# Performance work log

Hardware: AMD Instinct MI355X
Metric: run time of the kernel (lower is better)

Reference implementation:

```python
import jax, jax.numpy as jnp
import numpy as np

E, H, V = 512, 1024, 32000
T_IN, T_DEC, B = 128, 128, 64
SOS = 1
WIPE_IDS = jnp.array([2, 3, 4])  # <EOS>, '\u56fe', '\u6298'


def gru_cell(x, h, Wih, Whh, bih, bhh):
    # torch nn.GRU cell math
    gi = x @ Wih.T + bih  # [B, 3H]
    gh = h @ Whh.T + bhh  # [B, 3H]
    i_r, i_z, i_n = jnp.split(gi, 3, axis=-1)
    h_r, h_z, h_n = jnp.split(gh, 3, axis=-1)
    r = jax.nn.sigmoid(i_r + h_r)
    z = jax.nn.sigmoid(i_z + h_z)
    n = jnp.tanh(i_n + r * h_n)
    return (1.0 - z) * n + z * h


def setup_inputs() -> dict:
    key = jax.random.key(0)
    ks = jax.random.split(key, 20)
    f = lambda k, shape: jax.random.normal(k, shape, jnp.float32) * 0.05
    inp = {
        'emb': f(ks[0], (V, E)),
        'enc_Wih': f(ks[1], (3 * H, E)), 'enc_Whh': f(ks[2], (3 * H, H)),
        'enc_bih': f(ks[3], (3 * H,)), 'enc_bhh': f(ks[4], (3 * H,)),
        'attn_W': f(ks[5], (T_IN, E + H)), 'attn_b': f(ks[6], (T_IN,)),
        'comb_W': f(ks[7], (H, E + H)), 'comb_b': f(ks[8], (H,)),
        'dec_Wih': f(ks[9], (3 * H, H)), 'dec_Whh': f(ks[10], (3 * H, H)),
        'dec_bih': f(ks[11], (3 * H,)), 'dec_bhh': f(ks[12], (3 * H,)),
        'out_W': f(ks[13], (V, H)), 'out_b': f(ks[14], (V,)),
        'src_tokens': jax.random.randint(ks[15], (B, T_IN), 0, V, jnp.int32),
        'tgt_tokens': jax.random.randint(ks[16], (B, T_DEC), 0, V, jnp.int32),
    }
    # pack_padded_sequence needs lengths sorted descending with max == T_IN
    sl = jax.random.randint(ks[17], (B,), 1, T_IN + 1, jnp.int32).at[0].set(T_IN)
    inp['src_lengths'] = jnp.sort(sl)[::-1]
    tl = jax.random.randint(ks[18], (B,), 1, T_DEC + 1, jnp.int32).at[0].set(T_DEC)
    inp['tgt_lengths'] = tl
    return inp


def reference(emb, enc_Wih, enc_Whh, enc_bih, enc_bhh, attn_W, attn_b,
              comb_W, comb_b, dec_Wih, dec_Whh, dec_bih, dec_bhh,
              out_W, out_b, src_tokens, src_lengths, tgt_tokens, tgt_lengths):
    # ---------------- Encoder (packed GRU semantics) ----------------
    x = emb[src_tokens]  # [B, T_IN, E]  (dropout is eval-mode identity)
    valid = jnp.arange(T_IN)[None, :] < src_lengths[:, None]  # [B, T_IN]

    def enc_step(h, inp):
        xt, vt = inp  # [B,E], [B]
        hn = gru_cell(xt, h, enc_Wih, enc_Whh, enc_bih, enc_bhh)
        h = jnp.where(vt[:, None], hn, h)          # freeze hidden past length
        out = jnp.where(vt[:, None], hn, 0.0)      # pad_packed zeros past length
        return h, out

    h0 = jnp.zeros((B, H), emb.dtype)
    enc_h, enc_out = jax.lax.scan(enc_step, h0, (x.transpose(1, 0, 2), valid.T))
    enc_out = enc_out.transpose(1, 0, 2)  # [B, T_IN, H]
    enc_out = jax.nn.log_softmax(enc_out, axis=1)  # LogSoftmax(dim=1) over time, as in source

    # ---------------- Attention decoder with teacher forcing ----------------
    sos = jnp.full((B,), SOS, src_tokens.dtype)

    def dec_step(carry, inp):
        h, prev = carry
        di, tgt_t = inp
        e = emb[prev]  # [B, E]
        union = jnp.concatenate([e, h], axis=-1)  # [B, E+H]
        aw = jax.nn.softmax(union @ attn_W.T + attn_b, axis=-1)  # [B, T_IN]
        info = jnp.einsum('bt,bth->bh', aw, enc_out)  # bmm
        comb = jax.nn.relu(jnp.concatenate([e, info], axis=-1) @ comb_W.T + comb_b)
        h = gru_cell(comb, h, dec_Wih, dec_Whh, dec_bih, dec_bhh)
        logits = h @ out_W.T + out_b  # [B, V]
        m = di < tgt_lengths  # [B] wipeEOS condition: now_len < length[i]
        wiped = jnp.where(m[:, None], 0.0, logits[:, WIPE_IDS])
        logits = logits.at[:, WIPE_IDS].set(wiped)
        pred_t = jnp.argmax(logits, axis=-1)
        ce = -jax.nn.log_softmax(logits, axis=-1)[jnp.arange(B), tgt_t]
        mf = m.astype(logits.dtype)
        step_loss = jnp.sum(ce * mf) / jnp.sum(mf)  # masked_select(...).mean()
        return (h, tgt_t), (pred_t, step_loss)

    (_, _), (preds, losses) = jax.lax.scan(
        dec_step, (enc_h, sos), (jnp.arange(T_DEC), tgt_tokens.T))
    return preds.T, jnp.sum(losses)
```

## Files before the change

### kernel.cpp

```cpp
#include <hip/hip_runtime.h>
#include <math.h>

typedef long long i64;

#define B_    64
#define TIN   128
#define TDEC  128
#define E_    512
#define H_    1024
#define V_    32000
#define H3    3072
#define EH    1536
#define NROWS 8192
#define BH    (B_ * H_)

__device__ inline unsigned int ordf(float v) {
  unsigned int u = __float_as_uint(v);
  return (u & 0x80000000u) ? ~u : (u | 0x80000000u);
}

__device__ __forceinline__ void fma16(float acc[4][4], float4 s, float4 w) {
  acc[0][0] = fmaf(s.x, w.x, acc[0][0]); acc[0][1] = fmaf(s.x, w.y, acc[0][1]);
  acc[0][2] = fmaf(s.x, w.z, acc[0][2]); acc[0][3] = fmaf(s.x, w.w, acc[0][3]);
  acc[1][0] = fmaf(s.y, w.x, acc[1][0]); acc[1][1] = fmaf(s.y, w.y, acc[1][1]);
  acc[1][2] = fmaf(s.y, w.z, acc[1][2]); acc[1][3] = fmaf(s.y, w.w, acc[1][3]);
  acc[2][0] = fmaf(s.z, w.x, acc[2][0]); acc[2][1] = fmaf(s.z, w.y, acc[2][1]);
  acc[2][2] = fmaf(s.z, w.z, acc[2][2]); acc[2][3] = fmaf(s.z, w.w, acc[2][3]);
  acc[3][0] = fmaf(s.w, w.x, acc[3][0]); acc[3][1] = fmaf(s.w, w.y, acc[3][1]);
  acc[3][2] = fmaf(s.w, w.z, acc[3][2]); acc[3][3] = fmaf(s.w, w.w, acc[3][3]);
}

__global__ void diag_fill(float* __restrict__ out, int n, float val) {
  int i = blockIdx.x * blockDim.x + threadIdx.x;
  if (i < n) out[i] = val;
}

__global__ void init_ws(float* __restrict__ hbuf, unsigned long long* __restrict__ amaxkey,
                        float* __restrict__ sumexp) {
  int i = blockIdx.x * blockDim.x + threadIdx.x;
  if (i < 2 * B_ * H_) hbuf[i] = 0.f;
  if (i < NROWS) { amaxkey[i] = 0ull; sumexp[i] = 0.f; }
}

__global__ void prep_tokens(const int* __restrict__ src, const int* __restrict__ tgt,
                            int* __restrict__ tok_src, int* __restrict__ tok_prev) {
  int r = blockIdx.x * blockDim.x + threadIdx.x;
  if (r >= NROWS) return;
  int t = r >> 6, b = r & 63;
  tok_src[r]  = src[b * TIN + t];
  tok_prev[r] = (t == 0) ? 1 : tgt[b * TDEC + (t - 1)];
}

__global__ __launch_bounds__(256)
void gemm_gather(const float* __restrict__ emb, const int* __restrict__ tok,
                 const float* __restrict__ W, int wstride,
                 const float* __restrict__ bias,
                 float* __restrict__ C, int ldc) {
  __shared__ float As[32][132];
  __shared__ float Bs[32][136];
  __shared__ int toks[128];
  const int tid = threadIdx.x;
  const int tx = tid & 15, ty = tid >> 4;
  const int r0 = blockIdx.y * 128, n0 = blockIdx.x * 128;
  if (tid < 128) toks[tid] = tok[r0 + tid];
  __syncthreads();
  float acc[8][8];
#pragma unroll
  for (int i = 0; i < 8; ++i)
#pragma unroll
    for (int j = 0; j < 8; ++j) acc[i][j] = 0.f;

  for (int k0 = 0; k0 < E_; k0 += 32) {
#pragma unroll
    for (int j = 0; j < 4; ++j) {
      int s = tid + 256 * j;
      int m = s >> 3, k4 = (s & 7) << 2;
      float4 v = *reinterpret_cast<const float4*>(&emb[(i64)toks[m] * E_ + k0 + k4]);
      As[k4 + 0][m] = v.x; As[k4 + 1][m] = v.y; As[k4 + 2][m] = v.z; As[k4 + 3][m] = v.w;
      float4 u = *reinterpret_cast<const float4*>(&W[(i64)(n0 + m) * wstride + k0 + k4]);
      Bs[k4 + 0][m] = u.x; Bs[k4 + 1][m] = u.y; Bs[k4 + 2][m] = u.z; Bs[k4 + 3][m] = u.w;
    }
    __syncthreads();
#pragma unroll
    for (int k = 0; k < 32; ++k) {
      float a[8], b[8];
      *(float4*)&a[0] = *(float4*)&As[k][ty * 4];
      *(float4*)&a[4] = *(float4*)&As[k][64 + ty * 4];
      *(float4*)&b[0] = *(float4*)&Bs[k][tx * 4];
      *(float4*)&b[4] = *(float4*)&Bs[k][64 + tx * 4];
#pragma unroll
      for (int i = 0; i < 8; ++i)
#pragma unroll
        for (int j = 0; j < 8; ++j)
          acc[i][j] = fmaf(a[i], b[j], acc[i][j]);
    }
    __syncthreads();
  }
#pragma unroll
  for (int i = 0; i < 8; ++i) {
    int rl = (i < 4) ? (ty * 4 + i) : (64 + ty * 4 + i - 4);
    int r = r0 + rl;
#pragma unroll
    for (int j = 0; j < 8; ++j) {
      int cl = (j < 4) ? (tx * 4 + j) : (64 + tx * 4 + j - 4);
      int c = n0 + cl;
      C[(i64)r * ldc + c] = acc[i][j] + bias[c];
    }
  }
}

__global__ __launch_bounds__(512)
void enc_step2(const float* __restrict__ h_prev, float* __restrict__ h_next,
               const float* __restrict__ emb, const int* __restrict__ tokS,
               const float* __restrict__ Wih, const float* __restrict__ Whh,
               const float* __restrict__ bih, const float* __restrict__ bhh,
               const int* __restrict__ src_len, float* __restrict__ EncRaw, int t) {
  __shared__ float S[64][68];
  __shared__ float WL[64 * 32];
  __shared__ float red[8 * 1024];
  __shared__ int toks[64];
  const int tid = threadIdx.x;
  const int n0 = blockIdx.x * 4;
  const int bg = tid & 15, ac = (tid >> 4) & 3, ks = tid >> 6;
  const int b0 = bg * 4;
  if (tid < 64) toks[tid] = tokS[t * B_ + tid];
  float acc[4][4] = {{0}};
  for (int ch = 0; ch < 24; ++ch) {
    const bool isE = ch < 8;
    const int k0 = (isE ? ch : ch - 8) * 64;
    __syncthreads();
    {
      int b = tid & 63, kb = (tid >> 6) * 8;
      const float* src = isE ? &emb[(i64)toks[b] * E_ + k0 + kb]
                             : &h_prev[(i64)b * H_ + k0 + kb];
      float4 v0 = *(const float4*)src;
      float4 v1 = *(const float4*)(src + 4);
      S[kb + 0][b] = v0.x; S[kb + 1][b] = v0.y; S[kb + 2][b] = v0.z; S[kb + 3][b] = v0.w;
      S[kb + 4][b] = v1.x; S[kb + 5][b] = v1.y; S[kb + 6][b] = v1.z; S[kb + 7][b] = v1.w;
    }
    if (tid < 192) {
      int lin = tid * 4;
      int row12 = lin >> 6, k4 = lin & 63;
      int m = row12 >> 2, c = row12 & 3;
      const float* W = isE ? Wih : Whh;
      const int K = isE ? E_ : H_;
      float4 w = *(const float4*)&W[(i64)(m * H_ + n0 + c) * K + k0 + k4];
      int slot = ((m ^ ((k4 >> 2) & 7)) << 2) + c;
      WL[(k4 + 0) * 32 + slot] = w.x;
      WL[(k4 + 1) * 32 + slot] = w.y;
      WL[(k4 + 2) * 32 + slot] = w.z;
      WL[(k4 + 3) * 32 + slot] = w.w;
    }
    __syncthreads();
    const bool active = (ac < 2) || (ac == 2 && isE) || (ac == 3 && !isE);
    if (active) {
      const int m = (ac < 2) ? ac : 2;
#pragma unroll
      for (int kk = ks * 8; kk < ks * 8 + 8; ++kk) {
        float4 sv = *(float4*)&S[kk][b0];
        float4 wv = *(float4*)&WL[kk * 32 + ((m ^ ((kk >> 2) & 7)) << 2)];
        fma16(acc, sv, wv);
      }
    }
  }
  __syncthreads();
#pragma unroll
  for (int bi = 0; bi < 4; ++bi)
#pragma unroll
    for (int c = 0; c < 4; ++c)
      red[ks * 1024 + ac * 256 + c * 64 + b0 + bi] = acc[bi][c];
  __syncthreads();
  if (tid < 256) {
    int b = tid & 63, c = tid >> 6, col = n0 + c;
    float sr = 0, sz = 0, gin = 0, ghn = 0;
#pragma unroll
    for (int k2 = 0; k2 < 8; ++k2) {
      sr  += red[k2 * 1024 +   0 + c * 64 + b];
      sz  += red[k2 * 1024 + 256 + c * 64 + b];
      gin += red[k2 * 1024 + 512 + c * 64 + b];
      ghn += red[k2 * 1024 + 768 + c * 64 + b];
    }
    float r = 1.f / (1.f + expf(-(sr + bih[col] + bhh[col])));
    float z = 1.f / (1.f + expf(-(sz + bih[H_ + col] + bhh[H_ + col])));
    float nn = tanhf(gin + bih[2 * H_ + col] + r * (ghn + bhh[2 * H_ + col]));
    float hpv = h_prev[(i64)b * H_ + col];
    float hnew = (1.f - z) * nn + z * hpv;
    bool valid = t < src_len[b];
    h_next[(i64)b * H_ + col] = valid ? hnew : hpv;
    EncRaw[((i64)b * TIN + t) * H_ + col] = valid ? hnew : 0.f;
  }
}

__global__ void ls_time(float* __restrict__ Enc) {
  int idx = blockIdx.x * blockDim.x + threadIdx.x;
  int b = idx >> 10, c = idx & 1023;
  const i64 base = (i64)b * TIN * H_ + c;
  float M = -INFINITY;
  for (int t = 0; t < TIN; ++t) M = fmaxf(M, Enc[base + (i64)t * H_]);
  float S = 0.f;
  for (int t = 0; t < TIN; ++t) S += expf(Enc[base + (i64)t * H_] - M);
  float lg = M + logf(S);
  for (int t = 0; t < TIN; ++t) Enc[base + (i64)t * H_] -= lg;
}

__global__ __launch_bounds__(512)
void attn_info2(const float* __restrict__ h_prev, const float* __restrict__ Ae,
                const float* __restrict__ attn_W, const float* __restrict__ EncLS,
                float* __restrict__ info, int t) {
  __shared__ float hl[H_];
  __shared__ float sc[TIN];
  __shared__ float inf2[512];
  const int b = blockIdx.x & 63, quarter = blockIdx.x >> 6;
  const int tid = threadIdx.x;
  if (tid < 256) {
    float4 v = *(const float4*)&h_prev[(i64)b * H_ + tid * 4];
    *(float4*)&hl[tid * 4] = v;
  }
  __syncthreads();
  const int w = tid >> 6, lane = tid & 63;
#pragma unroll
  for (int si = 0; si < 16; ++si) {
    int s = w * 16 + si;
    float p = 0.f;
#pragma unroll
    for (int jj = 0; jj < 16; ++jj) {
      int j = jj * 64 + lane;
      p = fmaf(hl[j], attn_W[(i64)s * EH + E_ + j], p);
    }
#pragma unroll
    for (int off = 32; off > 0; off >>= 1) p += __shfl_down(p, off);
    if (lane == 0) sc[s] = p + Ae[((i64)t * B_ + b) * TIN + s];
  }
  __syncthreads();
  if (tid < 64) {
    float v0 = sc[tid], v1 = sc[tid + 64];
    float mx = fmaxf(v0, v1);
#pragma unroll
    for (int off = 32; off > 0; off >>= 1) mx = fmaxf(mx, __shfl_xor(mx, off));
    float e0 = expf(v0 - mx), e1 = expf(v1 - mx);
    float ss = e0 + e1;
#pragma unroll
    for (int off = 32; off > 0; off >>= 1) ss += __shfl_xor(ss, off);
    sc[tid] = e0 / ss; sc[tid + 64] = e1 / ss;
  }
  __syncthreads();
  {
    int c = quarter * 256 + (tid & 255);
    int th = tid >> 8;
    float acc = 0.f;
    for (int t2 = th * 64; t2 < th * 64 + 64; ++t2)
      acc = fmaf(sc[t2], EncLS[((i64)b * TIN + t2) * H_ + c], acc);
    inf2[tid] = acc;
    __syncthreads();
    if (th == 0) info[(i64)b * H_ + c] = acc + inf2[tid + 256];
  }
}

__global__ __launch_bounds__(512)
void comb2(const float* __restrict__ info, const float* __restrict__ emb,
           const int* __restrict__ tokP, const float* __restrict__ comb_W,
           const float* __restrict__ comb_b, float* __restrict__ comb, int t) {
  __shared__ float S[64][68];
  __shared__ float WB[64 * 20];
  __shared__ float red[8 * 256];
  __shared__ int toks[64];
  const int tid = threadIdx.x;
  const int n0 = blockIdx.x * 4;
  const int bg = tid & 15, cs = (tid >> 4) & 3, ks = tid >> 6;
  const int b0 = bg * 4;
  if (tid < 64) toks[tid] = tokP[t * B_ + tid];
  float acc[4] = {0, 0, 0, 0};
  for (int ch = 0; ch < 24; ++ch) {
    const bool isE = ch < 8;
    const int k0 = (isE ? ch : ch - 8) * 64;
    __syncthreads();
    {
      int b = tid & 63, kb = (tid >> 6) * 8;
      const float* src = isE ? &emb[(i64)toks[b] * E_ + k0 + kb]
                             : &info[(i64)b * H_ + k0 + kb];
      float4 v0 = *(const float4*)src;
      float4 v1 = *(const float4*)(src + 4);
      S[kb + 0][b] = v0.x; S[kb + 1][b] = v0.y; S[kb + 2][b] = v0.z; S[kb + 3][b] = v0.w;
      S[kb + 4][b] = v1.x; S[kb + 5][b] = v1.y; S[kb + 6][b] = v1.z; S[kb + 7][b] = v1.w;
    }
    if (tid < 64) {
      int k = tid;
      i64 koff = (i64)(isE ? 0 : E_) + k0 + k;
      float4 w;
      w.x = comb_W[(i64)(n0 + 0) * EH + koff];
      w.y = comb_W[(i64)(n0 + 1) * EH + koff];
      w.z = comb_W[(i64)(n0 + 2) * EH + koff];
      w.w = comb_W[(i64)(n0 + 3) * EH + koff];
      *(float4*)&WB[k * 20] = w;
    }
    __syncthreads();
#pragma unroll
    for (int kk = ks * 8; kk < ks * 8 + 8; ++kk) {
      float4 sv = *(float4*)&S[kk][b0];
      float wv = WB[kk * 20 + cs];
      acc[0] = fmaf(sv.x, wv, acc[0]);
      acc[1] = fmaf(sv.y, wv, acc[1]);
      acc[2] = fmaf(sv.z, wv, acc[2]);
      acc[3] = fmaf(sv.w, wv, acc[3]);
    }
  }
  __syncthreads();
#pragma unroll
  for (int bi = 0; bi < 4; ++bi)
    red[ks * 256 + cs * 64 + b0 + bi] = acc[bi];
  __syncthreads();
  if (tid < 256) {
    int b = tid & 63, c = tid >> 6;
    float s = comb_b[n0 + c];
#pragma unroll
    for (int k2 = 0; k2 < 8; ++k2) s += red[k2 * 256 + c * 64 + b];
    comb[(i64)b * H_ + n0 + c] = fmaxf(s, 0.f);
  }
}

__global__ __launch_bounds__(512)
void dec_gru2(const float* __restrict__ h_prev, const float* __restrict__ comb,
              const float* __restrict__ Wih, const float* __restrict__ Whh,
              const float* __restrict__ bih, const float* __restrict__ bhh,
              float* __restrict__ h_out) {
  __shared__ float S1[64][68];
  __shared__ float S2[64][68];
  __shared__ float WL[64 * 32];
  __shared__ float red[8 * 1024];
  const int tid = threadIdx.x;
  const int n0 = blockIdx.x * 4;
  const int bg = tid & 15, ac = (tid >> 4) & 3, ks = tid >> 6;
  const int b0 = bg * 4;
  float acc[4][4] = {{0}};
  for (int ch = 0; ch < 16; ++ch) {
    const int k0 = ch * 64;
    __syncthreads();
    {
      int b = tid & 63, kb = (tid >> 6) * 8;
      const float* s1 = &h_prev[(i64)b * H_ + k0 + kb];
      const float* s2 = &comb[(i64)b * H_ + k0 + kb];
      float4 v0 = *(const float4*)s1, v1 = *(const float4*)(s1 + 4);
      S1[kb + 0][b] = v0.x; S1[kb + 1][b] = v0.y; S1[kb + 2][b] = v0.z; S1[kb + 3][b] = v0.w;
      S1[kb + 4][b] = v1.x; S1[kb + 5][b] = v1.y; S1[kb + 6][b] = v1.z; S1[kb + 7][b] = v1.w;
      float4 u0 = *(const float4*)s2, u1 = *(const float4*)(s2 + 4);
      S2[kb + 0][b] = u0.x; S2[kb + 1][b] = u0.y; S2[kb + 2][b] = u0.z; S2[kb + 3][b] = u0.w;
      S2[kb + 4][b] = u1.x; S2[kb + 5][b] = u1.y; S2[kb + 6][b] = u1.z; S2[kb + 7][b] = u1.w;
    }
    if (tid < 384) {
      int lin = tid * 4;
      int row24 = lin >> 6, k4 = lin & 63;
      int m = row24 >> 2, c = row24 & 3;
      int g = m >> 1;
      const float* W = (m & 1) ? Wih : Whh;
      float4 w = *(const float4*)&W[(i64)(g * H_ + n0 + c) * H_ + k0 + k4];
      int slot = ((m ^ ((k4 >> 2) & 7)) << 2) + c;
      WL[(k4 + 0) * 32 + slot] = w.x;
      WL[(k4 + 1) * 32 + slot] = w.y;
      WL[(k4 + 2) * 32 + slot] = w.z;
      WL[(k4 + 3) * 32 + slot] = w.w;
    }
    __syncthreads();
    if (ac < 2) {
#pragma unroll
      for (int kk = ks * 8; kk < ks * 8 + 8; ++kk) {
        int key = (kk >> 2) & 7;
        float4 h4 = *(float4*)&S1[kk][b0];
        float4 c4 = *(float4*)&S2[kk][b0];
        float4 wh = *(float4*)&WL[kk * 32 + (((2 * ac) ^ key) << 2)];
        float4 wi = *(float4*)&WL[kk * 32 + (((2 * ac + 1) ^ key) << 2)];
        fma16(acc, h4, wh);
        fma16(acc, c4, wi);
      }
    } else if (ac == 2) {
#pragma unroll
      for (int kk = ks * 8; kk < ks * 8 + 8; ++kk) {
        int key = (kk >> 2) & 7;
        float4 c4 = *(float4*)&S2[kk][b0];
        float4 wi = *(float4*)&WL[kk * 32 + ((5 ^ key) << 2)];
        fma16(acc, c4, wi);
      }
    } else {
#pragma unroll
      for (int kk = ks * 8; kk < ks * 8 + 8; ++kk) {
        int key = (kk >> 2) & 7;
        float4 h4 = *(float4*)&S1[kk][b0];
        float4 wh = *(float4*)&WL[kk * 32 + ((4 ^ key) << 2)];
        fma16(acc, h4, wh);
      }
    }
  }
  __syncthreads();
#pragma unroll
  for (int bi = 0; bi < 4; ++bi)
#pragma unroll
    for (int c = 0; c < 4; ++c)
      red[ks * 1024 + ac * 256 + c * 64 + b0 + bi] = acc[bi][c];
  __syncthreads();
  if (tid < 256) {
    int b = tid & 63, c = tid >> 6, col = n0 + c;
    float sr = 0, sz = 0, gin = 0, ghn = 0;
#pragma unroll
    for (int k2 = 0; k2 < 8; ++k2) {
      sr  += red[k2 * 1024 +   0 + c * 64 + b];
      sz  += red[k2 * 1024 + 256 + c * 64 + b];
      gin += red[k2 * 1024 + 512 + c * 64 + b];
      ghn += red[k2 * 1024 + 768 + c * 64 + b];
    }
    float r = 1.f / (1.f + expf(-(sr + bih[col] + bhh[col])));
    float z = 1.f / (1.f + expf(-(sz + bih[H_ + col] + bhh[H_ + col])));
    float nn = tanhf(gin + bih[2 * H_ + col] + r * (ghn + bhh[2 * H_ + col]));
    float hpv = h_prev[(i64)b * H_ + col];
    h_out[(i64)b * H_ + col] = (1.f - z) * nn + z * hpv;
  }
}

__global__ __launch_bounds__(256)
void logits_fused(const float* __restrict__ A, const float* __restrict__ Wout,
                  const float* __restrict__ outb, const int* __restrict__ tlen,
                  unsigned long long* __restrict__ amaxkey, float* __restrict__ sumexp) {
  __shared__ union {
    struct { float As[32][132]; float Bs[32][136]; } g;
    struct { float redm[128][17]; int redi[128][17]; float reds[128][17]; } r;
  } sh;
  const int tid = threadIdx.x;
  const int tx = tid & 15, ty = tid >> 4;
  const int r0 = blockIdx.y * 128, n0 = blockIdx.x * 128;
  float acc[8][8];
#pragma unroll
  for (int i = 0; i < 8; ++i)
#pragma unroll
    for (int j = 0; j < 8; ++j) acc[i][j] = 0.f;

  for (int k0 = 0; k0 < H_; k0 += 32) {
#pragma unroll
    for (int j = 0; j < 4; ++j) {
      int s = tid + 256 * j;
      int m = s >> 3, k4 = (s & 7) << 2;
      float4 v = *reinterpret_cast<const float4*>(&A[(i64)(r0 + m) * H_ + k0 + k4]);
      sh.g.As[k4 + 0][m] = v.x; sh.g.As[k4 + 1][m] = v.y;
      sh.g.As[k4 + 2][m] = v.z; sh.g.As[k4 + 3][m] = v.w;
      float4 u = *reinterpret_cast<const float4*>(&Wout[(i64)(n0 + m) * H_ + k0 + k4]);
      sh.g.Bs[k4 + 0][m] = u.x; sh.g.Bs[k4 + 1][m] = u.y;
      sh.g.Bs[k4 + 2][m] = u.z; sh.g.Bs[k4 + 3][m] = u.w;
    }
    __syncthreads();
#pragma unroll
    for (int k = 0; k < 32; ++k) {
      float a[8], b[8];
      *(float4*)&a[0] = *(float4*)&sh.g.As[k][ty * 4];
      *(float4*)&a[4] = *(float4*)&sh.g.As[k][64 + ty * 4];
      *(float4*)&b[0] = *(float4*)&sh.g.Bs[k][tx * 4];
      *(float4*)&b[4] = *(float4*)&sh.g.Bs[k][64 + tx * 4];
#pragma unroll
      for (int i = 0; i < 8; ++i)
#pragma unroll
        for (int j = 0; j < 8; ++j)
          acc[i][j] = fmaf(a[i], b[j], acc[i][j]);
    }
    __syncthreads();
  }

  int cols[8], rloc[8];
#pragma unroll
  for (int j = 0; j < 8; ++j) cols[j] = n0 + ((j < 4) ? (tx * 4 + j) : (64 + tx * 4 + j - 4));
#pragma unroll
  for (int i = 0; i < 8; ++i) rloc[i] = (i < 4) ? (ty * 4 + i) : (64 + ty * 4 + i - 4);

#pragma unroll
  for (int i = 0; i < 8; ++i) {
    int r = r0 + rloc[i];
    int t = r >> 6, b = r & 63;
    bool m = t < tlen[b];
    float lm = -INFINITY; int li = 0x7fffffff; float ls = 0.f;
#pragma unroll
    for (int j = 0; j < 8; ++j) {
      float v = acc[i][j] + outb[cols[j]];
      if (m && cols[j] >= 2 && cols[j] <= 4) v = 0.f;
      ls += expf(v);
      if (v > lm || (v == lm && cols[j] < li)) { lm = v; li = cols[j]; }
    }
    sh.r.redm[rloc[i]][tx] = lm; sh.r.redi[rloc[i]][tx] = li; sh.r.reds[rloc[i]][tx] = ls;
  }
  __syncthreads();
  if (tid < 128) {
    float M = -INFINITY; int I = 0x7fffffff; float S = 0.f;
#pragma unroll
    for (int x = 0; x < 16; ++x) {
      float v = sh.r.redm[tid][x]; int id = sh.r.redi[tid][x];
      if (v > M || (v == M && id < I)) { M = v; I = id; }
      S += sh.r.reds[tid][x];
    }
    unsigned long long key = ((unsigned long long)ordf(M) << 32) | (0xFFFFFFFFu - (unsigned)I);
    atomicMax(&amaxkey[r0 + tid], key);
    atomicAdd(&sumexp[r0 + tid], S);
  }
}

__global__ void tlogit_kernel(const float* __restrict__ Hd, const float* __restrict__ Wout,
                              const float* __restrict__ outb, const int* __restrict__ tgt,
                              const int* __restrict__ tlen, float* __restrict__ tlog) {
  const int tid = threadIdx.x;
  const int w = tid >> 6, lane = tid & 63;
  const int r = blockIdx.x * 4 + w;
  const int t = r >> 6, b = r & 63;
  const int tg = tgt[b * TDEC + t];
  float p = 0.f;
#pragma unroll
  for (int jj = 0; jj < 16; ++jj) {
    int j = jj * 64 + lane;
    p = fmaf(Hd[(i64)r * H_ + j], Wout[(i64)tg * H_ + j], p);
  }
#pragma unroll
  for (int off = 32; off > 0; off >>= 1) p += __shfl_down(p, off);
  if (lane == 0) {
    float v = p + outb[tg];
    if ((t < tlen[b]) && tg >= 2 && tg <= 4) v = 0.f;
    tlog[r] = v;
  }
}

__global__ void merge_kernel(const unsigned long long* __restrict__ amaxkey,
                             const float* __restrict__ sumexp,
                             const float* __restrict__ tlog,
                             const int* __restrict__ tlen,
                             float* __restrict__ out, float* __restrict__ loss_t) {
  const int t = blockIdx.x, b = threadIdx.x;
  const int r = t * 64 + b;
  unsigned long long key = amaxkey[r];
  int I = (int)(0xFFFFFFFFu - (unsigned)(key & 0xFFFFFFFFull));
  float lse = logf(sumexp[r]);
  float ce = lse - tlog[r];
  bool m = t < tlen[b];
  out[b * TDEC + t] = (float)I;
  float num = m ? ce : 0.f;
  float den = m ? 1.f : 0.f;
#pragma unroll
  for (int off = 32; off > 0; off >>= 1) {
    num += __shfl_down(num, off);
    den += __shfl_down(den, off);
  }
  if (b == 0) loss_t[t] = num / den;
}

__global__ void loss_sum(const float* __restrict__ loss_t, float* __restrict__ out) {
  const int tid = threadIdx.x;
  float v = loss_t[tid];
#pragma unroll
  for (int off = 32; off > 0; off >>= 1) v += __shfl_down(v, off);
  __shared__ float ps[2];
  if ((tid & 63) == 0) ps[tid >> 6] = v;
  __syncthreads();
  if (tid == 0) out[B_ * TDEC] = ps[0] + ps[1];
}

extern "C" void kernel_launch(void* const* d_in, const int* in_sizes, int n_in,
                              void* d_out, int out_size, void* d_ws, size_t ws_size,
                              hipStream_t stream) {
  const float* emb     = (const float*)d_in[0];
  const float* enc_Wih = (const float*)d_in[1];
  const float* enc_Whh = (const float*)d_in[2];
  const float* enc_bih = (const float*)d_in[3];
  const float* enc_bhh = (const float*)d_in[4];
  const float* attn_W  = (const float*)d_in[5];
  const float* attn_b  = (const float*)d_in[6];
  const float* comb_W  = (const float*)d_in[7];
  const float* comb_b  = (const float*)d_in[8];
  const float* dec_Wih = (const float*)d_in[9];
  const float* dec_Whh = (const float*)d_in[10];
  const float* dec_bih = (const float*)d_in[11];
  const float* dec_bhh = (const float*)d_in[12];
  const float* out_W   = (const float*)d_in[13];
  const float* out_b   = (const float*)d_in[14];
  const int* src_tok = (const int*)d_in[15];
  const int* tgt_tok;
  const int* src_len;
  const int* tgt_len;
  if (in_sizes[16] == B_ * TDEC) {
    tgt_tok = (const int*)d_in[16];
    src_len = (const int*)d_in[17];
    tgt_len = (const int*)d_in[18];
  } else {
    src_len = (const int*)d_in[16];
    tgt_len = (const int*)d_in[17];
    tgt_tok = (const int*)d_in[18];
  }
  float* out = (float*)d_out;
  char* wsb = (char*)d_ws;
  size_t off = 0;
  auto alloc = [&](size_t bytes) { void* p = wsb + off; off += (bytes + 255) & ~(size_t)255; return p; };

  float* EncLS = (float*)alloc((size_t)NROWS * H_ * 4);
  float* hbuf  = (float*)alloc(2ull * B_ * H_ * 4);
  float* Ae    = (float*)alloc((size_t)NROWS * TIN * 4);
  float* Hdec  = (float*)alloc((size_t)NROWS * H_ * 4);
  float* info  = (float*)alloc((size_t)B_ * H_ * 4);
  float* comb  = (float*)alloc((size_t)B_ * H_ * 4);
  unsigned long long* amaxkey = (unsigned long long*)alloc((size_t)NROWS * 8);
  float* sumexp = (float*)alloc((size_t)NROWS * 4);
  float* tlog  = (float*)alloc((size_t)NROWS * 4);
  float* lossT = (float*)alloc(TDEC * 4);
  int* tokS    = (int*)alloc(NROWS * 4);
  int* tokP    = (int*)alloc(NROWS * 4);

  if (off > ws_size) {
    diag_fill<<<(out_size + 255) / 256, 256, 0, stream>>>(out, out_size, (float)ws_size);
    return;
  }

  init_ws<<<512, 256, 0, stream>>>(hbuf, amaxkey, sumexp);
  prep_tokens<<<32, 256, 0, stream>>>(src_tok, tgt_tok, tokS, tokP);
  gemm_gather<<<dim3(1, 64), 256, 0, stream>>>(emb, tokP, attn_W, EH, attn_b, Ae, TIN);

  for (int t = 0; t < TIN; ++t) {
    const float* hp = hbuf + (size_t)(t & 1) * BH;
    float* hn = hbuf + (size_t)((t + 1) & 1) * BH;
    enc_step2<<<256, 512, 0, stream>>>(hp, hn, emb, tokS, enc_Wih, enc_Whh,
                                       enc_bih, enc_bhh, src_len, EncLS, t);
  }
  ls_time<<<256, 256, 0, stream>>>(EncLS);

  for (int t = 0; t < TDEC; ++t) {
    const float* hp = (t == 0) ? hbuf : (Hdec + (i64)(t - 1) * BH);
    attn_info2<<<256, 512, 0, stream>>>(hp, Ae, attn_W, EncLS, info, t);
    comb2<<<256, 512, 0, stream>>>(info, emb, tokP, comb_W, comb_b, comb, t);
    dec_gru2<<<256, 512, 0, stream>>>(hp, comb, dec_Wih, dec_Whh, dec_bih, dec_bhh,
                                      Hdec + (i64)t * BH);
  }

  logits_fused<<<dim3(250, 64), 256, 0, stream>>>(Hdec, out_W, out_b, tgt_len, amaxkey, sumexp);
  tlogit_kernel<<<2048, 256, 0, stream>>>(Hdec, out_W, out_b, tgt_tok, tgt_len, tlog);
  merge_kernel<<<128, 64, 0, stream>>>(amaxkey, sumexp, tlog, tgt_len, out, lossT);
  loss_sum<<<1, 128, 0, stream>>>(lossT, out);
}
```

Before: 36.11 ms.

## Precompute embedding part of combine projection as batched GEMM; union shared memory

The embedding half of the comb_W projection depends only on teacher-forced tokens, so it is computed once for all decoder steps by a batched gather-GEMM into a workspace buffer Ce. Each per-step comb2 launch then covers only the info half (16 chunks instead of 24) and adds the precomputed value. Shared-memory arrays in the step kernels are overlaid with unions to cut LDS usage, and nontemporal loads are used for EncLS and out_W streams. This costs an extra 32MB workspace buffer and one upfront GEMM, and falls back to the old path if the workspace is too small.

```diff
diff --git a/kernel.cpp b/kernel.cpp
--- a/kernel.cpp
+++ b/kernel.cpp
@@ -2,6 +2,7 @@
 #include <math.h>
 
 typedef long long i64;
+typedef float f32x4 __attribute__((ext_vector_type(4)));
 
 #define B_    64
 #define TIN   128
@@ -115,15 +116,15 @@
                const float* __restrict__ Wih, const float* __restrict__ Whh,
                const float* __restrict__ bih, const float* __restrict__ bhh,
                const int* __restrict__ src_len, float* __restrict__ EncRaw, int t) {
-  __shared__ float S[64][68];
-  __shared__ float WL[64 * 32];
-  __shared__ float red[8 * 1024];
-  __shared__ int toks[64];
+  __shared__ union {
+    struct { float S[64][68]; float WL[64 * 32]; int toks[64]; } m;
+    float red[8 * 1024];
+  } sh;
   const int tid = threadIdx.x;
   const int n0 = blockIdx.x * 4;
   const int bg = tid & 15, ac = (tid >> 4) & 3, ks = tid >> 6;
   const int b0 = bg * 4;
-  if (tid < 64) toks[tid] = tokS[t * B_ + tid];
+  if (tid < 64) sh.m.toks[tid] = tokS[t * B_ + tid];
   float acc[4][4] = {{0}};
   for (int ch = 0; ch < 24; ++ch) {
     const bool isE = ch < 8;
@@ -131,12 +132,14 @@
     __syncthreads();
     {
       int b = tid & 63, kb = (tid >> 6) * 8;
-      const float* src = isE ? &emb[(i64)toks[b] * E_ + k0 + kb]
+      const float* src = isE ? &emb[(i64)sh.m.toks[b] * E_ + k0 + kb]
                              : &h_prev[(i64)b * H_ + k0 + kb];
       float4 v0 = *(const float4*)src;
       float4 v1 = *(const float4*)(src + 4);
-      S[kb + 0][b] = v0.x; S[kb + 1][b] = v0.y; S[kb + 2][b] = v0.z; S[kb + 3][b] = v0.w;
-      S[kb + 4][b] = v1.x; S[kb + 5][b] = v1.y; S[kb + 6][b] = v1.z; S[kb + 7][b] = v1.w;
+      sh.m.S[kb + 0][b] = v0.x; sh.m.S[kb + 1][b] = v0.y;
+      sh.m.S[kb + 2][b] = v0.z; sh.m.S[kb + 3][b] = v0.w;
+      sh.m.S[kb + 4][b] = v1.x; sh.m.S[kb + 5][b] = v1.y;
+      sh.m.S[kb + 6][b] = v1.z; sh.m.S[kb + 7][b] = v1.w;
     }
     if (tid < 192) {
       int lin = tid * 4;
@@ -146,10 +149,10 @@
       const int K = isE ? E_ : H_;
       float4 w = *(const float4*)&W[(i64)(m * H_ + n0 + c) * K + k0 + k4];
       int slot = ((m ^ ((k4 >> 2) & 7)) << 2) + c;
-      WL[(k4 + 0) * 32 + slot] = w.x;
-      WL[(k4 + 1) * 32 + slot] = w.y;
-      WL[(k4 + 2) * 32 + slot] = w.z;
-      WL[(k4 + 3) * 32 + slot] = w.w;
+      sh.m.WL[(k4 + 0) * 32 + slot] = w.x;
+      sh.m.WL[(k4 + 1) * 32 + slot] = w.y;
+      sh.m.WL[(k4 + 2) * 32 + slot] = w.z;
+      sh.m.WL[(k4 + 3) * 32 + slot] = w.w;
     }
     __syncthreads();
     const bool active = (ac < 2) || (ac == 2 && isE) || (ac == 3 && !isE);
@@ -157,8 +160,8 @@
       const int m = (ac < 2) ? ac : 2;
 #pragma unroll
       for (int kk = ks * 8; kk < ks * 8 + 8; ++kk) {
-        float4 sv = *(float4*)&S[kk][b0];
-        float4 wv = *(float4*)&WL[kk * 32 + ((m ^ ((kk >> 2) & 7)) << 2)];
+        float4 sv = *(float4*)&sh.m.S[kk][b0];
+        float4 wv = *(float4*)&sh.m.WL[kk * 32 + ((m ^ ((kk >> 2) & 7)) << 2)];
         fma16(acc, sv, wv);
       }
     }
@@ -168,17 +171,17 @@
   for (int bi = 0; bi < 4; ++bi)
 #pragma unroll
     for (int c = 0; c < 4; ++c)
-      red[ks * 1024 + ac * 256 + c * 64 + b0 + bi] = acc[bi][c];
+      sh.red[ks * 1024 + ac * 256 + c * 64 + b0 + bi] = acc[bi][c];
   __syncthreads();
   if (tid < 256) {
     int b = tid & 63, c = tid >> 6, col = n0 + c;
     float sr = 0, sz = 0, gin = 0, ghn = 0;
 #pragma unroll
     for (int k2 = 0; k2 < 8; ++k2) {
-      sr  += red[k2 * 1024 +   0 + c * 64 + b];
-      sz  += red[k2 * 1024 + 256 + c * 64 + b];
-      gin += red[k2 * 1024 + 512 + c * 64 + b];
-      ghn += red[k2 * 1024 + 768 + c * 64 + b];
+      sr  += sh.red[k2 * 1024 +   0 + c * 64 + b];
+      sz  += sh.red[k2 * 1024 + 256 + c * 64 + b];
+      gin += sh.red[k2 * 1024 + 512 + c * 64 + b];
+      ghn += sh.red[k2 * 1024 + 768 + c * 64 + b];
     }
     float r = 1.f / (1.f + expf(-(sr + bih[col] + bhh[col])));
     float z = 1.f / (1.f + expf(-(sz + bih[H_ + col] + bhh[H_ + col])));
@@ -248,40 +251,47 @@
     int c = quarter * 256 + (tid & 255);
     int th = tid >> 8;
     float acc = 0.f;
-    for (int t2 = th * 64; t2 < th * 64 + 64; ++t2)
-      acc = fmaf(sc[t2], EncLS[((i64)b * TIN + t2) * H_ + c], acc);
+    for (int t2 = th * 64; t2 < th * 64 + 64; ++t2) {
+      float ev = __builtin_nontemporal_load(&EncLS[((i64)b * TIN + t2) * H_ + c]);
+      acc = fmaf(sc[t2], ev, acc);
+    }
     inf2[tid] = acc;
     __syncthreads();
     if (th == 0) info[(i64)b * H_ + c] = acc + inf2[tid + 256];
   }
 }
 
+template<int MODE>
 __global__ __launch_bounds__(512)
 void comb2(const float* __restrict__ info, const float* __restrict__ emb,
            const int* __restrict__ tokP, const float* __restrict__ comb_W,
-           const float* __restrict__ comb_b, float* __restrict__ comb, int t) {
-  __shared__ float S[64][68];
-  __shared__ float WB[64 * 20];
-  __shared__ float red[8 * 256];
-  __shared__ int toks[64];
+           const float* __restrict__ comb_b, const float* __restrict__ Ce,
+           float* __restrict__ comb, int t) {
+  __shared__ union {
+    struct { float S[64][68]; float WB[64 * 20]; int toks[64]; } m;
+    float red[8 * 256];
+  } sh;
   const int tid = threadIdx.x;
   const int n0 = blockIdx.x * 4;
   const int bg = tid & 15, cs = (tid >> 4) & 3, ks = tid >> 6;
   const int b0 = bg * 4;
-  if (tid < 64) toks[tid] = tokP[t * B_ + tid];
+  if (MODE == 1 && tid < 64) sh.m.toks[tid] = tokP[t * B_ + tid];
   float acc[4] = {0, 0, 0, 0};
-  for (int ch = 0; ch < 24; ++ch) {
-    const bool isE = ch < 8;
-    const int k0 = (isE ? ch : ch - 8) * 64;
+  const int NCH = (MODE == 1) ? 24 : 16;
+  for (int ch = 0; ch < NCH; ++ch) {
+    const bool isE = (MODE == 1) && (ch < 8);
+    const int k0 = (isE ? ch : (MODE == 1 ? ch - 8 : ch)) * 64;
     __syncthreads();
     {
       int b = tid & 63, kb = (tid >> 6) * 8;
-      const float* src = isE ? &emb[(i64)toks[b] * E_ + k0 + kb]
+      const float* src = isE ? &emb[(i64)sh.m.toks[b] * E_ + k0 + kb]
                              : &info[(i64)b * H_ + k0 + kb];
       float4 v0 = *(const float4*)src;
       float4 v1 = *(const float4*)(src + 4);
-      S[kb + 0][b] = v0.x; S[kb + 1][b] = v0.y; S[kb + 2][b] = v0.z; S[kb + 3][b] = v0.w;
-      S[kb + 4][b] = v1.x; S[kb + 5][b] = v1.y; S[kb + 6][b] = v1.z; S[kb + 7][b] = v1.w;
+      sh.m.S[kb + 0][b] = v0.x; sh.m.S[kb + 1][b] = v0.y;
+      sh.m.S[kb + 2][b] = v0.z; sh.m.S[kb + 3][b] = v0.w;
+      sh.m.S[kb + 4][b] = v1.x; sh.m.S[kb + 5][b] = v1.y;
+      sh.m.S[kb + 6][b] = v1.z; sh.m.S[kb + 7][b] = v1.w;
     }
     if (tid < 64) {
       int k = tid;
@@ -291,13 +301,13 @@
       w.y = comb_W[(i64)(n0 + 1) * EH + koff];
       w.z = comb_W[(i64)(n0 + 2) * EH + koff];
       w.w = comb_W[(i64)(n0 + 3) * EH + koff];
-      *(float4*)&WB[k * 20] = w;
+      *(float4*)&sh.m.WB[k * 20] = w;
     }
     __syncthreads();
 #pragma unroll
     for (int kk = ks * 8; kk < ks * 8 + 8; ++kk) {
-      float4 sv = *(float4*)&S[kk][b0];
-      float wv = WB[kk * 20 + cs];
+      float4 sv = *(float4*)&sh.m.S[kk][b0];
+      float wv = sh.m.WB[kk * 20 + cs];
       acc[0] = fmaf(sv.x, wv, acc[0]);
       acc[1] = fmaf(sv.y, wv, acc[1]);
       acc[2] = fmaf(sv.z, wv, acc[2]);
@@ -307,13 +317,14 @@
   __syncthreads();
 #pragma unroll
   for (int bi = 0; bi < 4; ++bi)
-    red[ks * 256 + cs * 64 + b0 + bi] = acc[bi];
+    sh.red[ks * 256 + cs * 64 + b0 + bi] = acc[bi];
   __syncthreads();
   if (tid < 256) {
     int b = tid & 63, c = tid >> 6;
-    float s = comb_b[n0 + c];
-#pragma unroll
-    for (int k2 = 0; k2 < 8; ++k2) s += red[k2 * 256 + c * 64 + b];
+    float base = (MODE == 0) ? Ce[((i64)t * B_ + b) * H_ + n0 + c] : comb_b[n0 + c];
+    float s = base;
+#pragma unroll
+    for (int k2 = 0; k2 < 8; ++k2) s += sh.red[k2 * 256 + c * 64 + b];
     comb[(i64)b * H_ + n0 + c] = fmaxf(s, 0.f);
   }
 }
@@ -323,10 +334,10 @@
               const float* __restrict__ Wih, const float* __restrict__ Whh,
               const float* __restrict__ bih, const float* __restrict__ bhh,
               float* __restrict__ h_out) {
-  __shared__ float S1[64][68];
-  __shared__ float S2[64][68];
-  __shared__ float WL[64 * 32];
-  __shared__ float red[8 * 1024];
+  __shared__ union {
+    struct { float S1[64][68]; float S2[64][68]; float WL[64 * 32]; } m;
+    float red[8 * 1024];
+  } sh;
   const int tid = threadIdx.x;
   const int n0 = blockIdx.x * 4;
   const int bg = tid & 15, ac = (tid >> 4) & 3, ks = tid >> 6;
@@ -340,11 +351,15 @@
       const float* s1 = &h_prev[(i64)b * H_ + k0 + kb];
       const float* s2 = &comb[(i64)b * H_ + k0 + kb];
       float4 v0 = *(const float4*)s1, v1 = *(const float4*)(s1 + 4);
-      S1[kb + 0][b] = v0.x; S1[kb + 1][b] = v0.y; S1[kb + 2][b] = v0.z; S1[kb + 3][b] = v0.w;
-      S1[kb + 4][b] = v1.x; S1[kb + 5][b] = v1.y; S1[kb + 6][b] = v1.z; S1[kb + 7][b] = v1.w;
+      sh.m.S1[kb + 0][b] = v0.x; sh.m.S1[kb + 1][b] = v0.y;
+      sh.m.S1[kb + 2][b] = v0.z; sh.m.S1[kb + 3][b] = v0.w;
+      sh.m.S1[kb + 4][b] = v1.x; sh.m.S1[kb + 5][b] = v1.y;
+      sh.m.S1[kb + 6][b] = v1.z; sh.m.S1[kb + 7][b] = v1.w;
       float4 u0 = *(const float4*)s2, u1 = *(const float4*)(s2 + 4);
-      S2[kb + 0][b] = u0.x; S2[kb + 1][b] = u0.y; S2[kb + 2][b] = u0.z; S2[kb + 3][b] = u0.w;
-      S2[kb + 4][b] = u1.x; S2[kb + 5][b] = u1.y; S2[kb + 6][b] = u1.z; S2[kb + 7][b] = u1.w;
+      sh.m.S2[kb + 0][b] = u0.x; sh.m.S2[kb + 1][b] = u0.y;
+      sh.m.S2[kb + 2][b] = u0.z; sh.m.S2[kb + 3][b] = u0.w;
+      sh.m.S2[kb + 4][b] = u1.x; sh.m.S2[kb + 5][b] = u1.y;
+      sh.m.S2[kb + 6][b] = u1.z; sh.m.S2[kb + 7][b] = u1.w;
     }
     if (tid < 384) {
       int lin = tid * 4;
@@ -354,20 +369,20 @@
       const float* W = (m & 1) ? Wih : Whh;
       float4 w = *(const float4*)&W[(i64)(g * H_ + n0 + c) * H_ + k0 + k4];
       int slot = ((m ^ ((k4 >> 2) & 7)) << 2) + c;
-      WL[(k4 + 0) * 32 + slot] = w.x;
-      WL[(k4 + 1) * 32 + slot] = w.y;
-      WL[(k4 + 2) * 32 + slot] = w.z;
-      WL[(k4 + 3) * 32 + slot] = w.w;
+      sh.m.WL[(k4 + 0) * 32 + slot] = w.x;
+      sh.m.WL[(k4 + 1) * 32 + slot] = w.y;
+      sh.m.WL[(k4 + 2) * 32 + slot] = w.z;
+      sh.m.WL[(k4 + 3) * 32 + slot] = w.w;
     }
     __syncthreads();
     if (ac < 2) {
 #pragma unroll
       for (int kk = ks * 8; kk < ks * 8 + 8; ++kk) {
         int key = (kk >> 2) & 7;
-        float4 h4 = *(float4*)&S1[kk][b0];
-        float4 c4 = *(float4*)&S2[kk][b0];
-        float4 wh = *(float4*)&WL[kk * 32 + (((2 * ac) ^ key) << 2)];
-        float4 wi = *(float4*)&WL[kk * 32 + (((2 * ac + 1) ^ key) << 2)];
+        float4 h4 = *(float4*)&sh.m.S1[kk][b0];
+        float4 c4 = *(float4*)&sh.m.S2[kk][b0];
+        float4 wh = *(float4*)&sh.m.WL[kk * 32 + (((2 * ac) ^ key) << 2)];
+        float4 wi = *(float4*)&sh.m.WL[kk * 32 + (((2 * ac + 1) ^ key) << 2)];
         fma16(acc, h4, wh);
         fma16(acc, c4, wi);
       }
@@ -375,16 +390,16 @@
 #pragma unroll
       for (int kk = ks * 8; kk < ks * 8 + 8; ++kk) {
         int key = (kk >> 2) & 7;
-        float4 c4 = *(float4*)&S2[kk][b0];
-        float4 wi = *(float4*)&WL[kk * 32 + ((5 ^ key) << 2)];
+        float4 c4 = *(float4*)&sh.m.S2[kk][b0];
+        float4 wi = *(float4*)&sh.m.WL[kk * 32 + ((5 ^ key) << 2)];
         fma16(acc, c4, wi);
       }
     } else {
 #pragma unroll
       for (int kk = ks * 8; kk < ks * 8 + 8; ++kk) {
         int key = (kk >> 2) & 7;
-        float4 h4 = *(float4*)&S1[kk][b0];
-        float4 wh = *(float4*)&WL[kk * 32 + ((4 ^ key) << 2)];
+        float4 h4 = *(float4*)&sh.m.S1[kk][b0];
+        float4 wh = *(float4*)&sh.m.WL[kk * 32 + ((4 ^ key) << 2)];
         fma16(acc, h4, wh);
       }
     }
@@ -394,17 +409,17 @@
   for (int bi = 0; bi < 4; ++bi)
 #pragma unroll
     for (int c = 0; c < 4; ++c)
-      red[ks * 1024 + ac * 256 + c * 64 + b0 + bi] = acc[bi][c];
+      sh.red[ks * 1024 + ac * 256 + c * 64 + b0 + bi] = acc[bi][c];
   __syncthreads();
   if (tid < 256) {
     int b = tid & 63, c = tid >> 6, col = n0 + c;
     float sr = 0, sz = 0, gin = 0, ghn = 0;
 #pragma unroll
     for (int k2 = 0; k2 < 8; ++k2) {
-      sr  += red[k2 * 1024 +   0 + c * 64 + b];
-      sz  += red[k2 * 1024 + 256 + c * 64 + b];
-      gin += red[k2 * 1024 + 512 + c * 64 + b];
-      ghn += red[k2 * 1024 + 768 + c * 64 + b];
+      sr  += sh.red[k2 * 1024 +   0 + c * 64 + b];
+      sz  += sh.red[k2 * 1024 + 256 + c * 64 + b];
+      gin += sh.red[k2 * 1024 + 512 + c * 64 + b];
+      ghn += sh.red[k2 * 1024 + 768 + c * 64 + b];
     }
     float r = 1.f / (1.f + expf(-(sr + bih[col] + bhh[col])));
     float z = 1.f / (1.f + expf(-(sz + bih[H_ + col] + bhh[H_ + col])));
@@ -439,7 +454,8 @@
       float4 v = *reinterpret_cast<const float4*>(&A[(i64)(r0 + m) * H_ + k0 + k4]);
       sh.g.As[k4 + 0][m] = v.x; sh.g.As[k4 + 1][m] = v.y;
       sh.g.As[k4 + 2][m] = v.z; sh.g.As[k4 + 3][m] = v.w;
-      float4 u = *reinterpret_cast<const float4*>(&Wout[(i64)(n0 + m) * H_ + k0 + k4]);
+      f32x4 u = __builtin_nontemporal_load(
+          reinterpret_cast<const f32x4*>(&Wout[(i64)(n0 + m) * H_ + k0 + k4]));
       sh.g.Bs[k4 + 0][m] = u.x; sh.g.Bs[k4 + 1][m] = u.y;
       sh.g.Bs[k4 + 2][m] = u.z; sh.g.Bs[k4 + 3][m] = u.w;
     }
@@ -607,9 +623,15 @@
     return;
   }
 
+  const size_t CeB = (size_t)NROWS * H_ * 4;
+  float* Ce = nullptr;
+  if (ws_size >= off + CeB + 256) Ce = (float*)alloc(CeB);
+
   init_ws<<<512, 256, 0, stream>>>(hbuf, amaxkey, sumexp);
   prep_tokens<<<32, 256, 0, stream>>>(src_tok, tgt_tok, tokS, tokP);
   gemm_gather<<<dim3(1, 64), 256, 0, stream>>>(emb, tokP, attn_W, EH, attn_b, Ae, TIN);
+  if (Ce)
+    gemm_gather<<<dim3(8, 64), 256, 0, stream>>>(emb, tokP, comb_W, EH, comb_b, Ce, H_);
 
   for (int t = 0; t < TIN; ++t) {
     const float* hp = hbuf + (size_t)(t & 1) * BH;
@@ -622,7 +644,10 @@
   for (int t = 0; t < TDEC; ++t) {
     const float* hp = (t == 0) ? hbuf : (Hdec + (i64)(t - 1) * BH);
     attn_info2<<<256, 512, 0, stream>>>(hp, Ae, attn_W, EncLS, info, t);
-    comb2<<<256, 512, 0, stream>>>(info, emb, tokP, comb_W, comb_b, comb, t);
+    if (Ce)
+      comb2<0><<<256, 512, 0, stream>>>(info, emb, tokP, comb_W, comb_b, Ce, comb, t);
+    else
+      comb2<1><<<256, 512, 0, stream>>>(info, emb, tokP, comb_W, comb_b, nullptr, comb, t);
     dec_gru2<<<256, 512, 0, stream>>>(hp, comb, dec_Wih, dec_Whh, dec_bih, dec_bhh,
                                       Hdec + (i64)t * BH);
   }
```

Measured after the change: 40.65 ms. 12.6% more time.
